# Optimization experiments

Measured on AMD Instinct MI355X. Metric: run time of the kernel, lower is better.

The kernel has to match this reference:

```python
import jax, jax.numpy as jnp
import numpy as np

B, N, E = 64, 1024, 16384
ZH, EF_DIM = 128, 64
RUP, RMAX, P = 10.0, 10.0, 6
MAX_ZVOCAB = 13   # max of z_embedding_dim=[13,4,8,6,6,8,2,4]
MAX_EFVOCAB = 8   # max of edge_features_embedding_dim=[6,3,3,8]


def setup_inputs() -> dict:
    key = jax.random.key(0)
    ks = jax.random.split(key, 9)
    z = jax.random.randint(ks[0], (B, N, 8), 0, 2)
    pos = jax.random.normal(ks[1], (B, N, 3), dtype=jnp.float32)
    idx_u = jax.random.randint(ks[2], (B, E), 0, N)
    # guarantee u != v so edge length > 0 almost surely
    idx_v = (idx_u + jax.random.randint(ks[3], (B, E), 1, N)) % N
    edge_index = jnp.stack([idx_u, idx_v], axis=1)  # (B,2,E)
    edge_features = jax.random.randint(ks[4], (B, E, 4), 0, 3)
    center_pos = jax.random.normal(ks[5], (B, N, 3), dtype=jnp.float32)
    # embedding tables padded to max vocab (unused rows never indexed)
    z_tables = jax.random.normal(ks[6], (8, MAX_ZVOCAB, ZH), dtype=jnp.float32)
    ef_tables = jax.random.normal(ks[7], (4, MAX_EFVOCAB, EF_DIM), dtype=jnp.float32)
    dV_table = jax.random.normal(ks[8], (3, EF_DIM), dtype=jnp.float32)
    return dict(z=z, pos=pos, edge_index=edge_index, edge_features=edge_features,
                center_pos=center_pos, z_tables=z_tables, ef_tables=ef_tables,
                dV_table=dV_table)


def _gather_nodes(x, idx):
    # x: (B,N,D), idx: (B,E) -> (B,E,D)
    return jnp.take_along_axis(x, idx[..., None], axis=1)


def reference(z, pos, edge_index, edge_features, center_pos, z_tables, ef_tables, dV_table):
    # node embedding: z_emb[0] + sum_{i=2..6} z_emb[i] (indices 1 and 7 unused, per source)
    emb1 = z_tables[0][z[..., 0]]
    for i in range(2, 7):
        emb1 = emb1 + z_tables[i][z[..., i]]

    idx_u, idx_v = edge_index[:, 0], edge_index[:, 1]
    posu = _gather_nodes(pos, idx_u)           # (B,E,3)
    posv = _gather_nodes(pos, idx_v)
    ev = posu - posv
    el = jnp.sqrt(jnp.maximum(jnp.sum(ev * ev, axis=-1, keepdims=True), 1e-24))  # (B,E,1)

    # Gaussian RBF over [0, rbound_upper]
    offsets = jnp.linspace(0.0, RUP, EF_DIM, dtype=jnp.float32)
    coeff = -0.5 / (offsets[1] - offsets[0]) ** 2
    ef = jnp.exp(coeff * (el - offsets) ** 2)  # (B,E,EF_DIM)

    for i in range(4):
        ef = ef + ef_tables[i][edge_features[..., i]]

    # dV sign branch (center_pos provided)
    center_pad = _gather_nodes(center_pos, idx_v)
    ecross = jnp.cross(posu, posv)
    dV = jnp.sum(ecross * center_pad, axis=-1)            # (B,E)
    dV_sign = jnp.sign(dV).astype(jnp.int32) + 1          # in {0,1,2}
    ef = ef * dV_table[dV_sign]

    # smooth polynomial envelope (DimeNet-style), zero beyond r_max
    x = el / RMAX
    env = (1.0 - 0.5 * (P + 1) * (P + 2) * x ** P
           + P * (P + 2) * x ** (P + 1)
           - 0.5 * P * (P + 1) * x ** (P + 2))
    env = jnp.where(x < 1.0, env, 0.0)
    ef = ef * env
    return emb1, ef
```

## Files before the change

### kernel.cpp

```cpp
#include <hip/hip_runtime.h>

#define BATCH   64
#define NNODE   1024
#define NEDGE   16384
#define ZHDIM   128
#define EFDIM   64
#define MAXZV   13
#define MAXEFV  8
#define NEDGES_TOT (BATCH * NEDGE)
#define NCOMBO  4096
#define AROWS   (NCOMBO * 3)

#define WS_A_OFF_FLOATS      0
#define WS_SCAL_OFF_FLOATS   (1024 * 1024)

__global__ __launch_bounds__(256) void combine_tables_kernel(
    const float* __restrict__ ef_tables,
    const float* __restrict__ dV_table,
    float*       __restrict__ A)
{
    int tid = blockIdx.x * 256 + threadIdx.x;
    int row = tid >> 4;
    int c4  = tid & 15;
    int combo = row / 3;
    int s     = row - combo * 3;
    int f3 = combo & 7, f2 = (combo >> 3) & 7, f1 = (combo >> 6) & 7, f0 = (combo >> 9) & 7;

    const float4* T = (const float4*)ef_tables;
    float4 t0 = T[(0 * MAXEFV + f0) * 16 + c4];
    float4 t1 = T[(1 * MAXEFV + f1) * 16 + c4];
    float4 t2 = T[(2 * MAXEFV + f2) * 16 + c4];
    float4 t3 = T[(3 * MAXEFV + f3) * 16 + c4];
    float4 dv = ((const float4*)dV_table)[s * 16 + c4];

    float4 o;
    o.x = (t0.x + t1.x + t2.x + t3.x) * dv.x;
    o.y = (t0.y + t1.y + t2.y + t3.y) * dv.y;
    o.z = (t0.z + t1.z + t2.z + t3.z) * dv.z;
    o.w = (t0.w + t1.w + t2.w + t3.w) * dv.w;
    ((float4*)A)[row * 16 + c4] = o;
}

__global__ __launch_bounds__(256) void edge_scalar_kernel(
    const float* __restrict__ pos,
    const int*   __restrict__ edge_index,
    const int*   __restrict__ edge_features,
    const float* __restrict__ center_pos,
    float4*      __restrict__ scal)
{
    int edge = blockIdx.x * 256 + threadIdx.x;
    int b = edge >> 14;
    int e = edge & (NEDGE - 1);

    int iu = edge_index[(b * 2 + 0) * NEDGE + e];
    int iv = edge_index[(b * 2 + 1) * NEDGE + e];

    const float* pu = pos + (size_t)(b * NNODE + iu) * 3;
    const float* pv = pos + (size_t)(b * NNODE + iv) * 3;
    float ux = pu[0], uy = pu[1], uz = pu[2];
    float vx = pv[0], vy = pv[1], vz = pv[2];

    float dx = ux - vx, dy = uy - vy, dz = uz - vz;
    float el = sqrtf(fmaxf(dx * dx + dy * dy + dz * dz, 1e-24f));

    float cx = uy * vz - uz * vy;
    float cy = uz * vx - ux * vz;
    float cz = ux * vy - uy * vx;
    const float* cp = center_pos + (size_t)(b * NNODE + iv) * 3;
    float dV = cx * cp[0] + cy * cp[1] + cz * cp[2];
    int sgn = (dV > 0.0f) ? 2 : ((dV < 0.0f) ? 0 : 1);

    float x  = el * 0.1f;
    float x3 = x * x * x;
    float x6 = x3 * x3;
    float env = 1.0f - 28.0f * x6 + 48.0f * x6 * x - 21.0f * x6 * x * x;
    env = (x < 1.0f) ? env : 0.0f;

    int4 f = ((const int4*)edge_features)[edge];
    int combo = ((f.x * 8 + f.y) * 8 + f.z) * 8 + f.w;
    int rowid = combo * 3 + sgn;

    float4 o;
    o.x = el;
    o.y = env;
    o.z = __int_as_float(rowid);
    o.w = __int_as_float(sgn);
    scal[edge] = o;
}

__global__ __launch_bounds__(256) void ef_expand_kernel(
    const float4* __restrict__ scal,
    const float*  __restrict__ A,
    const float*  __restrict__ dV_table,
    float*        __restrict__ out)
{
    int tid  = blockIdx.x * 256 + threadIdx.x;
    int edge = tid >> 4;
    int c4   = tid & 15;

    float4 sc = scal[edge];
    float el  = sc.x;
    float env = sc.y;
    int rowid = __float_as_int(sc.z);
    int sgn   = __float_as_int(sc.w);

    float4 a  = ((const float4*)A)[rowid * 16 + c4];
    float4 dv = ((const float4*)dV_table)[sgn * 16 + c4];

    const float step  = 10.0f / 63.0f;
    const float coeff = -0.5f / (step * step);

    float av[4]  = {a.x, a.y, a.z, a.w};
    float dvv[4] = {dv.x, dv.y, dv.z, dv.w};
    float r[4];
#pragma unroll
    for (int k = 0; k < 4; ++k) {
        int j = c4 * 4 + k;
        float d = el - step * (float)j;
        float g = expf(coeff * d * d);
        r[k] = fmaf(g, dvv[k], av[k]) * env;
    }

    float4 res;
    res.x = r[0]; res.y = r[1]; res.z = r[2]; res.w = r[3];
    ((float4*)out)[(size_t)edge * 16 + c4] = res;
}

__global__ __launch_bounds__(256) void emb1_kernel(
    const int*   __restrict__ z,
    const float* __restrict__ z_tables,
    float*       __restrict__ out)
{
    int tid  = blockIdx.x * 256 + threadIdx.x;
    int node = tid >> 5;
    int c4   = tid & 31;

    const int* zp = z + node * 8;
    int i0 = zp[0];
    int i2 = zp[2], i3 = zp[3], i4 = zp[4], i5 = zp[5], i6 = zp[6];

    const float4* t = (const float4*)z_tables;
    float4 a0 = t[(0 * MAXZV + i0) * 32 + c4];
    float4 a2 = t[(2 * MAXZV + i2) * 32 + c4];
    float4 a3 = t[(3 * MAXZV + i3) * 32 + c4];
    float4 a4 = t[(4 * MAXZV + i4) * 32 + c4];
    float4 a5 = t[(5 * MAXZV + i5) * 32 + c4];
    float4 a6 = t[(6 * MAXZV + i6) * 32 + c4];

    float4 s;
    s.x = a0.x + a2.x + a3.x + a4.x + a5.x + a6.x;
    s.y = a0.y + a2.y + a3.y + a4.y + a5.y + a6.y;
    s.z = a0.z + a2.z + a3.z + a4.z + a5.z + a6.z;
    s.w = a0.w + a2.w + a3.w + a4.w + a5.w + a6.w;

    ((float4*)out)[node * 32 + c4] = s;
}

extern "C" void kernel_launch(void* const* d_in, const int* in_sizes, int n_in,
                              void* d_out, int out_size, void* d_ws, size_t ws_size,
                              hipStream_t stream) {
    const int*   z             = (const int*)  d_in[0];
    const float* pos           = (const float*)d_in[1];
    const int*   edge_index    = (const int*)  d_in[2];
    const int*   edge_features = (const int*)  d_in[3];
    const float* center_pos    = (const float*)d_in[4];
    const float* z_tables      = (const float*)d_in[5];
    const float* ef_tables     = (const float*)d_in[6];
    const float* dV_table      = (const float*)d_in[7];

    float* out_emb1 = (float*)d_out;
    float* out_ef   = out_emb1 + (size_t)BATCH * NNODE * ZHDIM;

    float*  ws_A    = (float*)d_ws + WS_A_OFF_FLOATS;
    float4* ws_scal = (float4*)((float*)d_ws + WS_SCAL_OFF_FLOATS);

    combine_tables_kernel<<<AROWS * 16 / 256, 256, 0, stream>>>(ef_tables, dV_table, ws_A);

    edge_scalar_kernel<<<NEDGES_TOT / 256, 256, 0, stream>>>(
        pos, edge_index, edge_features, center_pos, ws_scal);

    emb1_kernel<<<BATCH * NNODE * 32 / 256, 256, 0, stream>>>(z, z_tables, out_emb1);

    ef_expand_kernel<<<NEDGES_TOT * 16 / 256, 256, 0, stream>>>(
        ws_scal, ws_A, dV_table, out_ef);
}
```

Measured before the change: 354.7 us.

## Fuse edge scalar and expand kernels, use exp2 and nontemporal stores

Merges the per-edge scalar computation into the expansion kernel: the first 16 threads of each block compute the edge scalars into shared memory, then all 256 threads expand 64 features per edge. This drops a kernel launch and the workspace round-trip of the scalar buffer. It also replaces expf with exp2f using a prescaled constant and writes the outputs with nontemporal stores. In exchange, most threads sit idle behind a barrier while the 16 scalar threads perform dependent gathers.

After: 389.2 us. 1.1x slower.

```diff
diff --git a/kernel.cpp b/kernel.cpp
--- a/kernel.cpp
+++ b/kernel.cpp
@@ -10,9 +10,10 @@
 #define NEDGES_TOT (BATCH * NEDGE)
 #define NCOMBO  4096
 #define AROWS   (NCOMBO * 3)
+#define EDGES_PER_BLOCK 16
 
-#define WS_A_OFF_FLOATS      0
-#define WS_SCAL_OFF_FLOATS   (1024 * 1024)
+typedef float f32x4 __attribute__((ext_vector_type(4)));
+
 
 __global__ __launch_bounds__(256) void combine_tables_kernel(
     const float* __restrict__ ef_tables,
@@ -41,64 +42,67 @@
     ((float4*)A)[row * 16 + c4] = o;
 }
 
-__global__ __launch_bounds__(256) void edge_scalar_kernel(
+__global__ __launch_bounds__(256) void ef_fused_kernel(
     const float* __restrict__ pos,
     const int*   __restrict__ edge_index,
     const int*   __restrict__ edge_features,
     const float* __restrict__ center_pos,
-    float4*      __restrict__ scal)
+    const float* __restrict__ A,
+    const float* __restrict__ dV_table,
+    float*       __restrict__ out)
 {
-    int edge = blockIdx.x * 256 + threadIdx.x;
-    int b = edge >> 14;
-    int e = edge & (NEDGE - 1);
+    __shared__ float4 s_scal[EDGES_PER_BLOCK];
 
-    int iu = edge_index[(b * 2 + 0) * NEDGE + e];
-    int iv = edge_index[(b * 2 + 1) * NEDGE + e];
+    int t = threadIdx.x;
+    int blk = blockIdx.x;
 
-    const float* pu = pos + (size_t)(b * NNODE + iu) * 3;
-    const float* pv = pos + (size_t)(b * NNODE + iv) * 3;
-    float ux = pu[0], uy = pu[1], uz = pu[2];
-    float vx = pv[0], vy = pv[1], vz = pv[2];
+    if (t < EDGES_PER_BLOCK) {
+        int edge = blk * EDGES_PER_BLOCK + t;
+        int b = edge >> 14;
+        int e = edge & (NEDGE - 1);
 
-    float dx = ux - vx, dy = uy - vy, dz = uz - vz;
-    float el = sqrtf(fmaxf(dx * dx + dy * dy + dz * dz, 1e-24f));
+        int iu = edge_index[(b * 2 + 0) * NEDGE + e];
+        int iv = edge_index[(b * 2 + 1) * NEDGE + e];
 
-    float cx = uy * vz - uz * vy;
-    float cy = uz * vx - ux * vz;
-    float cz = ux * vy - uy * vx;
-    const float* cp = center_pos + (size_t)(b * NNODE + iv) * 3;
-    float dV = cx * cp[0] + cy * cp[1] + cz * cp[2];
-    int sgn = (dV > 0.0f) ? 2 : ((dV < 0.0f) ? 0 : 1);
+        const float* pu = pos + (size_t)(b * NNODE + iu) * 3;
+        const float* pv = pos + (size_t)(b * NNODE + iv) * 3;
+        float ux = pu[0], uy = pu[1], uz = pu[2];
+        float vx = pv[0], vy = pv[1], vz = pv[2];
 
-    float x  = el * 0.1f;
-    float x3 = x * x * x;
-    float x6 = x3 * x3;
-    float env = 1.0f - 28.0f * x6 + 48.0f * x6 * x - 21.0f * x6 * x * x;
-    env = (x < 1.0f) ? env : 0.0f;
+        float dx = ux - vx, dy = uy - vy, dz = uz - vz;
+        float el = sqrtf(fmaxf(dx * dx + dy * dy + dz * dz, 1e-24f));
 
-    int4 f = ((const int4*)edge_features)[edge];
-    int combo = ((f.x * 8 + f.y) * 8 + f.z) * 8 + f.w;
-    int rowid = combo * 3 + sgn;
+        float cx = uy * vz - uz * vy;
+        float cy = uz * vx - ux * vz;
+        float cz = ux * vy - uy * vx;
+        const float* cp = center_pos + (size_t)(b * NNODE + iv) * 3;
+        float dV = cx * cp[0] + cy * cp[1] + cz * cp[2];
+        int sgn = (dV > 0.0f) ? 2 : ((dV < 0.0f) ? 0 : 1);
 
-    float4 o;
-    o.x = el;
-    o.y = env;
-    o.z = __int_as_float(rowid);
-    o.w = __int_as_float(sgn);
-    scal[edge] = o;
-}
+        float x  = el * 0.1f;
+        float x3 = x * x * x;
+        float x6 = x3 * x3;
+        float env = 1.0f - 28.0f * x6 + 48.0f * x6 * x - 21.0f * x6 * x * x;
+        env = (x < 1.0f) ? env : 0.0f;
 
-__global__ __launch_bounds__(256) void ef_expand_kernel(
-    const float4* __restrict__ scal,
-    const float*  __restrict__ A,
-    const float*  __restrict__ dV_table,
-    float*        __restrict__ out)
-{
-    int tid  = blockIdx.x * 256 + threadIdx.x;
-    int edge = tid >> 4;
-    int c4   = tid & 15;
+        int4 f = ((const int4*)edge_features)[edge];
+        int combo = ((f.x * 8 + f.y) * 8 + f.z) * 8 + f.w;
+        int rowid = combo * 3 + sgn;
 
-    float4 sc = scal[edge];
+        float4 o;
+        o.x = el;
+        o.y = env;
+        o.z = __int_as_float(rowid);
+        o.w = __int_as_float(sgn);
+        s_scal[t] = o;
+    }
+    __syncthreads();
+
+    int g   = t >> 4;
+    int c4  = t & 15;
+    int edge = blk * EDGES_PER_BLOCK + g;
+
+    float4 sc = s_scal[g];
     float el  = sc.x;
     float env = sc.y;
     int rowid = __float_as_int(sc.z);
@@ -107,8 +111,8 @@
     float4 a  = ((const float4*)A)[rowid * 16 + c4];
     float4 dv = ((const float4*)dV_table)[sgn * 16 + c4];
 
-    const float step  = 10.0f / 63.0f;
-    const float coeff = -0.5f / (step * step);
+    const float step = 10.0f / 63.0f;
+    const float c2 = (-0.5f / (step * step)) * 1.44269504088896f;
 
     float av[4]  = {a.x, a.y, a.z, a.w};
     float dvv[4] = {dv.x, dv.y, dv.z, dv.w};
@@ -117,13 +121,12 @@
     for (int k = 0; k < 4; ++k) {
         int j = c4 * 4 + k;
         float d = el - step * (float)j;
-        float g = expf(coeff * d * d);
-        r[k] = fmaf(g, dvv[k], av[k]) * env;
+        float gs = exp2f(c2 * d * d);
+        r[k] = fmaf(gs, dvv[k], av[k]) * env;
     }
 
-    float4 res;
-    res.x = r[0]; res.y = r[1]; res.z = r[2]; res.w = r[3];
-    ((float4*)out)[(size_t)edge * 16 + c4] = res;
+    f32x4 res = {r[0], r[1], r[2], r[3]};
+    __builtin_nontemporal_store(res, (f32x4*)out + (size_t)edge * 16 + c4);
 }
 
 __global__ __launch_bounds__(256) void emb1_kernel(
@@ -147,13 +150,13 @@
     float4 a5 = t[(5 * MAXZV + i5) * 32 + c4];
     float4 a6 = t[(6 * MAXZV + i6) * 32 + c4];
 
-    float4 s;
+    f32x4 s;
     s.x = a0.x + a2.x + a3.x + a4.x + a5.x + a6.x;
     s.y = a0.y + a2.y + a3.y + a4.y + a5.y + a6.y;
     s.z = a0.z + a2.z + a3.z + a4.z + a5.z + a6.z;
     s.w = a0.w + a2.w + a3.w + a4.w + a5.w + a6.w;
 
-    ((float4*)out)[node * 32 + c4] = s;
+    __builtin_nontemporal_store(s, (f32x4*)out + node * 32 + c4);
 }
 
 extern "C" void kernel_launch(void* const* d_in, const int* in_sizes, int n_in,
@@ -171,16 +174,12 @@
     float* out_emb1 = (float*)d_out;
     float* out_ef   = out_emb1 + (size_t)BATCH * NNODE * ZHDIM;
 
-    float*  ws_A    = (float*)d_ws + WS_A_OFF_FLOATS;
-    float4* ws_scal = (float4*)((float*)d_ws + WS_SCAL_OFF_FLOATS);
+    float* ws_A = (float*)d_ws;
 
     combine_tables_kernel<<<AROWS * 16 / 256, 256, 0, stream>>>(ef_tables, dV_table, ws_A);
 
-    edge_scalar_kernel<<<NEDGES_TOT / 256, 256, 0, stream>>>(
-        pos, edge_index, edge_features, center_pos, ws_scal);
-
     emb1_kernel<<<BATCH * NNODE * 32 / 256, 256, 0, stream>>>(z, z_tables, out_emb1);
 
-    ef_expand_kernel<<<NEDGES_TOT * 16 / 256, 256, 0, stream>>>(
-        ws_scal, ws_A, dV_table, out_ef);
+    ef_fused_kernel<<<NEDGES_TOT / EDGES_PER_BLOCK, 256, 0, stream>>>(
+        pos, edge_index, edge_features, center_pos, ws_A, dV_table, out_ef);
 }
```
